# Kernel optimization log

Hardware: AMD Instinct MI355X
Metric: run time of the kernel (lower is better)

Reference implementation:

```python
import jax, jax.numpy as jnp
import numpy as np

N = 100000   # nodes
E = 1600000  # edges
D = 128      # input feature dim
H = 64       # hidden dim
G = 64       # graphs in batch


def setup_inputs() -> dict:
    key = jax.random.key(0)
    ks = jax.random.split(key, 12)
    x = jax.random.normal(ks[0], (N, D), dtype=jnp.float32)
    ei = jax.random.randint(ks[1], (2, E), 0, N, dtype=jnp.int32)
    ew = jax.random.uniform(ks[2], (E,), dtype=jnp.float32)
    b = jnp.sort(jax.random.randint(ks[3], (N,), 0, G, dtype=jnp.int32))
    s = 0.05
    W1 = jax.random.normal(ks[4], (D, H), jnp.float32) * s
    b1 = jnp.zeros((H,), jnp.float32)
    W2 = jax.random.normal(ks[5], (H, H), jnp.float32) * s
    b2 = jnp.zeros((H,), jnp.float32)
    Wm1 = jax.random.normal(ks[6], (H, 32), jnp.float32) * s
    bm1 = jnp.zeros((32,), jnp.float32)
    Wm2 = jax.random.normal(ks[7], (32, 1), jnp.float32) * s
    bm2 = jnp.zeros((1,), jnp.float32)
    return {"x": x, "ei": ei, "ew": ew, "b": b,
            "W1": W1, "b1": b1, "W2": W2, "b2": b2,
            "Wm1": Wm1, "bm1": bm1, "Wm2": Wm2, "bm2": bm2}


def _gcn_norm(ei, ew, n):
    # PyG gcn_norm with add_self_loops=True (self-loop weight 1)
    loops = jnp.arange(n, dtype=ei.dtype)
    row = jnp.concatenate([ei[0], loops])
    col = jnp.concatenate([ei[1], loops])
    w = jnp.concatenate([ew, jnp.ones((n,), ew.dtype)])
    deg = jax.ops.segment_sum(w, col, num_segments=n)
    dinv = jnp.where(deg > 0, jax.lax.rsqrt(deg), 0.0)
    norm = dinv[row] * w * dinv[col]  # [E+N]
    return row, col, norm


def _gcn_conv(x, W, bias, row, col, norm, n):
    h = x @ W                                   # [N,H] small GEMM
    msg = h[row] * norm[:, None]                # gather over edges
    return jax.ops.segment_sum(msg, col, num_segments=n) + bias


def reference(x, ei, ew, b, W1, b1, W2, b2, Wm1, bm1, Wm2, bm2):
    n = x.shape[0]
    row, col, norm = _gcn_norm(ei, ew, n)
    h = jax.nn.relu(_gcn_conv(x, W1, b1, row, col, norm, n))
    h = jax.nn.relu(_gcn_conv(h, W2, b2, row, col, norm, n))
    # global_mean_pool over batch vector b
    sums = jax.ops.segment_sum(h, b, num_segments=G)
    cnt = jax.ops.segment_sum(jnp.ones((n,), h.dtype), b, num_segments=G)
    pooled = sums / jnp.maximum(cnt, 1.0)[:, None]  # [G,H]
    # MLP head: Linear(H,32) -> ReLU -> Linear(32,1)
    return jax.nn.relu(pooled @ Wm1 + bm1) @ Wm2 + bm2
```

## Files before the change

kernel.cpp:

```cpp
#include <hip/hip_runtime.h>
#include <hip/hip_bf16.h>
#include <hip/hip_fp16.h>


#define DIMH 64
#define BSH 7
#define BSZ 128
#define NBUCK_MAX 1024
#define EPB 4096
#define ESTRIDE 3072
#define CSTRIDE 4096

typedef _Float16 v8h __attribute__((ext_vector_type(8)));
typedef float v4f __attribute__((ext_vector_type(4)));

__global__ __launch_bounds__(512) void k_part(const int* __restrict__ row,
                                              const int* __restrict__ col,
                                              const float* __restrict__ ew,
                                              int* __restrict__ cursor,
                                              unsigned long long* __restrict__ part,
                                              int E, int nbuck) {
    __shared__ int h[NBUCK_MAX];
    __shared__ int h2[NBUCK_MAX];
    __shared__ int st[NBUCK_MAX];
    for (int i = threadIdx.x; i < nbuck; i += 512) { h[i] = 0; h2[i] = 0; }
    __syncthreads();
    int ebeg = blockIdx.x * EPB;
    int eend = min(ebeg + EPB, E);
    for (int e = ebeg + threadIdx.x; e < eend; e += 512)
        atomicAdd(&h[col[e] >> BSH], 1);
    __syncthreads();
    for (int i = threadIdx.x; i < nbuck; i += 512) {
        int c = h[i];
        st[i] = c ? i * ESTRIDE + atomicAdd(&cursor[i], c) : 0;
    }
    __syncthreads();
    for (int e = ebeg + threadIdx.x; e < eend; e += 512) {
        int c = col[e];
        int b = c >> BSH;
        int r = atomicAdd(&h2[b], 1);
        int slot = st[b] + r;
        if (slot < (b + 1) * ESTRIDE) {
            unsigned long long rec =
                ((unsigned long long)__float_as_uint(ew[e]) << 32) |
                ((unsigned long long)(unsigned)row[e] << 8) |
                (unsigned)(c & (BSZ - 1));
            part[slot] = rec;
        }
    }
}

__global__ __launch_bounds__(256) void k_sortB(const unsigned long long* __restrict__ part,
                                               const int* __restrict__ cursor,
                                               int2* __restrict__ csr,
                                               unsigned* __restrict__ rp,
                                               float* __restrict__ dinv, int N) {
    __shared__ int cnt[BSZ];
    __shared__ int scn[BSZ];
    __shared__ int cur[BSZ];
    __shared__ float dg[BSZ];
    int b = blockIdx.x;
    int nb0 = b << BSH;
    int nn = min(BSZ, N - nb0);
    int tid = threadIdx.x;
    if (tid < BSZ) { cnt[tid] = 0; dg[tid] = 1.0f; }
    __syncthreads();
    int ebeg = b * ESTRIDE;
    int eend = ebeg + min(cursor[b], ESTRIDE);
    for (int e = ebeg + tid; e < eend; e += 256)
        atomicAdd(&cnt[(int)(part[e] & (BSZ - 1))], 1);
    __syncthreads();
    int pc = 0;
    if (tid < BSZ) pc = min((cnt[tid] + 15) & ~15, 496);
    if (tid < BSZ) scn[tid] = pc;
    __syncthreads();
    for (int o = 1; o < BSZ; o <<= 1) {
        int t = 0;
        if (tid >= o && tid < BSZ) t = scn[tid - o];
        __syncthreads();
        if (tid >= o && tid < BSZ) scn[tid] += t;
        __syncthreads();
    }
    int Pb = b * CSTRIDE;
    int pofs = 0;
    if (tid < BSZ) {
        pofs = scn[tid] - pc;
        cur[tid] = pofs;
        if (tid < nn)
            rp[nb0 + tid] = ((unsigned)(pc >> 4) << 26) | (unsigned)(Pb + pofs);
    }
    __syncthreads();
    for (int e = ebeg + tid; e < eend; e += 256) {
        unsigned long long rec = part[e];
        int cl = (int)(rec & (BSZ - 1));
        float w = __uint_as_float((unsigned)(rec >> 32));
        int slot = atomicAdd(&cur[cl], 1);
        csr[Pb + slot] = make_int2((int)((rec >> 8) & 0xFFFFFF), __float_as_int(w));
        atomicAdd(&dg[cl], w);
    }
    __syncthreads();
    if (tid < nn) {
        int c = min(cnt[tid], pc);
        for (int k = c; k < pc; k++)
            csr[Pb + pofs + k] = make_int2(nb0 + tid, 0);
        dinv[nb0 + tid] = rsqrtf(dg[tid]);
    }
}

__global__ __launch_bounds__(256) void k_gemm_mfma(const float* __restrict__ X,
                                                   const float* __restrict__ W,
                                                   const float* __restrict__ dinv,
                                                   __half* __restrict__ Y, int n) {
    __shared__ _Float16 Wh[128 * 64];
    int tid = threadIdx.x;
    for (int i = tid * 4; i < 128 * 64; i += 256 * 4) {
        float4 w = *(const float4*)&W[i];
        Wh[i]     = (_Float16)w.x;
        Wh[i + 1] = (_Float16)w.y;
        Wh[i + 2] = (_Float16)w.z;
        Wh[i + 3] = (_Float16)w.w;
    }
    __syncthreads();

    int wv = tid >> 6;
    int lane = tid & 63;
    int m = lane & 15;
    int quad = lane >> 4;
    int tile = blockIdx.x * 4 + wv;
    int ntiles = (n + 15) >> 4;
    if (tile >= ntiles) return;

    v8h bf[4][4];
#pragma unroll
    for (int nt = 0; nt < 4; nt++)
#pragma unroll
        for (int s = 0; s < 4; s++)
#pragma unroll
            for (int j = 0; j < 8; j++)
                bf[nt][s][j] = Wh[(s * 32 + quad * 8 + j) * 64 + nt * 16 + m];

    v4f acc[4];
#pragma unroll
    for (int nt = 0; nt < 4; nt++) acc[nt] = (v4f){0.f, 0.f, 0.f, 0.f};

    int row = min(tile * 16 + m, n - 1);
    const float* xr = X + (size_t)row * 128;
#pragma unroll
    for (int s = 0; s < 4; s++) {
        float4 lo = *(const float4*)&xr[s * 32 + quad * 8];
        float4 hi = *(const float4*)&xr[s * 32 + quad * 8 + 4];
        v8h af;
        af[0] = (_Float16)lo.x; af[1] = (_Float16)lo.y;
        af[2] = (_Float16)lo.z; af[3] = (_Float16)lo.w;
        af[4] = (_Float16)hi.x; af[5] = (_Float16)hi.y;
        af[6] = (_Float16)hi.z; af[7] = (_Float16)hi.w;
#pragma unroll
        for (int nt = 0; nt < 4; nt++)
            acc[nt] = __builtin_amdgcn_mfma_f32_16x16x32_f16(af, bf[nt][s], acc[nt], 0, 0, 0);
    }

#pragma unroll
    for (int r = 0; r < 4; r++) {
        int node = tile * 16 + quad * 4 + r;
        if (node < n) {
            float di = dinv[node];
#pragma unroll
            for (int nt = 0; nt < 4; nt++)
                Y[(size_t)node * DIMH + nt * 16 + m] = __float2half(di * acc[nt][r]);
        }
    }
}

__global__ __launch_bounds__(256) void k_agg1f(const __half* __restrict__ Hin,
                                               const unsigned* __restrict__ rp,
                                               const int2* __restrict__ csr,
                                               const float* __restrict__ dinv,
                                               const float* __restrict__ bias,
                                               const float* __restrict__ W2,
                                               __half* __restrict__ T2, int n) {
    __shared__ float W2s[DIMH * DIMH];
    __shared__ __align__(16) _Float16 hbuf[4][DIMH];
    int tid = threadIdx.x;
    for (int i = tid * 4; i < DIMH * DIMH; i += 256 * 4)
        *(float4*)&W2s[i] = *(const float4*)&W2[i];
    __syncthreads();

    int lane = tid & 63;
    int wv = tid >> 6;
    int q = lane >> 4;
    int fp = lane & 15;

    const uint2* H2 = (const uint2*)Hin;
    int ngroups = (n + 3) >> 2;
    for (int grp = blockIdx.x; grp < ngroups; grp += gridDim.x) {
        int node = grp * 4 + wv;
        if (node >= n) continue;
        unsigned pk = rp[node];
        int p = (int)(pk & 0x3FFFFFFu);
        int iters = (int)(pk >> 26);
        float a0 = 0.f, a1 = 0.f, a2 = 0.f, a3 = 0.f;
        if (q == 0) {
            uint2 su = H2[(size_t)node * 16 + fp];
            float2 f0 = __half22float2(*(__half2*)&su.x);
            float2 f1 = __half22float2(*(__half2*)&su.y);
            a0 = f0.x; a1 = f0.y; a2 = f1.x; a3 = f1.y;
        }
        int it = 0;
        for (; it + 2 <= iters; it += 2, p += 32) {
            int4 mA0 = *(const int4*)&csr[p + 2 * q];
            int4 mB0 = *(const int4*)&csr[p + 8 + 2 * q];
            int4 mA1 = *(const int4*)&csr[p + 16 + 2 * q];
            int4 mB1 = *(const int4*)&csr[p + 24 + 2 * q];
            uint2 u0 = H2[(size_t)mA0.x * 16 + fp];
            uint2 u1 = H2[(size_t)mA0.z * 16 + fp];
            uint2 u2 = H2[(size_t)mB0.x * 16 + fp];
            uint2 u3 = H2[(size_t)mB0.z * 16 + fp];
            uint2 u4 = H2[(size_t)mA1.x * 16 + fp];
            uint2 u5 = H2[(size_t)mA1.z * 16 + fp];
            uint2 u6 = H2[(size_t)mB1.x * 16 + fp];
            uint2 u7 = H2[(size_t)mB1.z * 16 + fp];
            float w0 = __int_as_float(mA0.y), w1 = __int_as_float(mA0.w);
            float w2 = __int_as_float(mB0.y), w3 = __int_as_float(mB0.w);
            float w4 = __int_as_float(mA1.y), w5 = __int_as_float(mA1.w);
            float w6 = __int_as_float(mB1.y), w7 = __int_as_float(mB1.w);
            float2 f;
            f = __half22float2(*(__half2*)&u0.x); a0 += w0 * f.x; a1 += w0 * f.y;
            f = __half22float2(*(__half2*)&u0.y); a2 += w0 * f.x; a3 += w0 * f.y;
            f = __half22float2(*(__half2*)&u1.x); a0 += w1 * f.x; a1 += w1 * f.y;
            f = __half22float2(*(__half2*)&u1.y); a2 += w1 * f.x; a3 += w1 * f.y;
            f = __half22float2(*(__half2*)&u2.x); a0 += w2 * f.x; a1 += w2 * f.y;
            f = __half22float2(*(__half2*)&u2.y); a2 += w2 * f.x; a3 += w2 * f.y;
            f = __half22float2(*(__half2*)&u3.x); a0 += w3 * f.x; a1 += w3 * f.y;
            f = __half22float2(*(__half2*)&u3.y); a2 += w3 * f.x; a3 += w3 * f.y;
            f = __half22float2(*(__half2*)&u4.x); a0 += w4 * f.x; a1 += w4 * f.y;
            f = __half22float2(*(__half2*)&u4.y); a2 += w4 * f.x; a3 += w4 * f.y;
            f = __half22float2(*(__half2*)&u5.x); a0 += w5 * f.x; a1 += w5 * f.y;
            f = __half22float2(*(__half2*)&u5.y); a2 += w5 * f.x; a3 += w5 * f.y;
            f = __half22float2(*(__half2*)&u6.x); a0 += w6 * f.x; a1 += w6 * f.y;
            f = __half22float2(*(__half2*)&u6.y); a2 += w6 * f.x; a3 += w6 * f.y;
            f = __half22float2(*(__half2*)&u7.x); a0 += w7 * f.x; a1 += w7 * f.y;
            f = __half22float2(*(__half2*)&u7.y); a2 += w7 * f.x; a3 += w7 * f.y;
        }
        if (it < iters) {
            int4 mA = *(const int4*)&csr[p + 2 * q];
            int4 mB = *(const int4*)&csr[p + 8 + 2 * q];
            uint2 u0 = H2[(size_t)mA.x * 16 + fp];
            uint2 u1 = H2[(size_t)mA.z * 16 + fp];
            uint2 u2 = H2[(size_t)mB.x * 16 + fp];
            uint2 u3 = H2[(size_t)mB.z * 16 + fp];
            float w0 = __int_as_float(mA.y), w1 = __int_as_float(mA.w);
            float w2 = __int_as_float(mB.y), w3 = __int_as_float(mB.w);
            float2 f;
            f = __half22float2(*(__half2*)&u0.x); a0 += w0 * f.x; a1 += w0 * f.y;
            f = __half22float2(*(__half2*)&u0.y); a2 += w0 * f.x; a3 += w0 * f.y;
            f = __half22float2(*(__half2*)&u1.x); a0 += w1 * f.x; a1 += w1 * f.y;
            f = __half22float2(*(__half2*)&u1.y); a2 += w1 * f.x; a3 += w1 * f.y;
            f = __half22float2(*(__half2*)&u2.x); a0 += w2 * f.x; a1 += w2 * f.y;
            f = __half22float2(*(__half2*)&u2.y); a2 += w2 * f.x; a3 += w2 * f.y;
            f = __half22float2(*(__half2*)&u3.x); a0 += w3 * f.x; a1 += w3 * f.y;
            f = __half22float2(*(__half2*)&u3.y); a2 += w3 * f.x; a3 += w3 * f.y;
        }
        a0 += __shfl_xor(a0, 16, 64); a0 += __shfl_xor(a0, 32, 64);
        a1 += __shfl_xor(a1, 16, 64); a1 += __shfl_xor(a1, 32, 64);
        a2 += __shfl_xor(a2, 16, 64); a2 += __shfl_xor(a2, 32, 64);
        a3 += __shfl_xor(a3, 16, 64); a3 += __shfl_xor(a3, 32, 64);
        float di = dinv[node];
        if (q == 0) {
            float4 bs = *(const float4*)&bias[fp * 4];
            float v0 = fmaxf(di * a0 + bs.x, 0.f);
            float v1 = fmaxf(di * a1 + bs.y, 0.f);
            float v2 = fmaxf(di * a2 + bs.z, 0.f);
            float v3 = fmaxf(di * a3 + bs.w, 0.f);
            __half2 h0 = __floats2half2_rn(v0, v1);
            __half2 h1 = __floats2half2_rn(v2, v3);
            uint2 o;
            o.x = *(unsigned*)&h0;
            o.y = *(unsigned*)&h1;
            *(uint2*)&hbuf[wv][fp * 4] = o;
        }
        float acc2 = 0.f;
        const unsigned* hb = (const unsigned*)hbuf[wv];
#pragma unroll
        for (int k8 = 0; k8 < 8; k8++) {
            uint4 hc = *(const uint4*)&hb[k8 * 4];
            float2 g0 = __half22float2(*(__half2*)&hc.x);
            float2 g1 = __half22float2(*(__half2*)&hc.y);
            float2 g2 = __half22float2(*(__half2*)&hc.z);
            float2 g3 = __half22float2(*(__half2*)&hc.w);
            const float* wc = &W2s[(k8 * 8) * DIMH + lane];
            acc2 += g0.x * wc[0 * DIMH] + g0.y * wc[1 * DIMH]
                  + g1.x * wc[2 * DIMH] + g1.y * wc[3 * DIMH]
                  + g2.x * wc[4 * DIMH] + g2.y * wc[5 * DIMH]
                  + g3.x * wc[6 * DIMH] + g3.y * wc[7 * DIMH];
        }
        T2[(size_t)node * DIMH + lane] = __float2half(di * acc2);
    }
}

__global__ __launch_bounds__(256) void k_aggN(const __half* __restrict__ Hin,
                                              const unsigned* __restrict__ rp,
                                              const int2* __restrict__ csr,
                                              const float* __restrict__ dinv,
                                              const float* __restrict__ bias,
                                              __half* __restrict__ Hout, int n) {
    int lane = threadIdx.x & 63;
    int wv = threadIdx.x >> 6;
    int node = blockIdx.x * 4 + wv;
    if (node >= n) return;
    unsigned pk = rp[node];
    int p = (int)(pk & 0x3FFFFFFu);
    int iters = (int)(pk >> 26);
    int q = lane >> 4;
    int fp = lane & 15;
    const uint2* H2 = (const uint2*)Hin;
    float a0 = 0.f, a1 = 0.f, a2 = 0.f, a3 = 0.f;
    if (q == 0) {
        uint2 su = H2[(size_t)node * 16 + fp];
        float2 f0 = __half22float2(*(__half2*)&su.x);
        float2 f1 = __half22float2(*(__half2*)&su.y);
        a0 = f0.x; a1 = f0.y; a2 = f1.x; a3 = f1.y;
    }
    int it = 0;
    for (; it + 2 <= iters; it += 2, p += 32) {
        int4 mA0 = *(const int4*)&csr[p + 2 * q];
        int4 mB0 = *(const int4*)&csr[p + 8 + 2 * q];
        int4 mA1 = *(const int4*)&csr[p + 16 + 2 * q];
        int4 mB1 = *(const int4*)&csr[p + 24 + 2 * q];
        uint2 u0 = H2[(size_t)mA0.x * 16 + fp];
        uint2 u1 = H2[(size_t)mA0.z * 16 + fp];
        uint2 u2 = H2[(size_t)mB0.x * 16 + fp];
        uint2 u3 = H2[(size_t)mB0.z * 16 + fp];
        uint2 u4 = H2[(size_t)mA1.x * 16 + fp];
        uint2 u5 = H2[(size_t)mA1.z * 16 + fp];
        uint2 u6 = H2[(size_t)mB1.x * 16 + fp];
        uint2 u7 = H2[(size_t)mB1.z * 16 + fp];
        float w0 = __int_as_float(mA0.y), w1 = __int_as_float(mA0.w);
        float w2 = __int_as_float(mB0.y), w3 = __int_as_float(mB0.w);
        float w4 = __int_as_float(mA1.y), w5 = __int_as_float(mA1.w);
        float w6 = __int_as_float(mB1.y), w7 = __int_as_float(mB1.w);
        float2 f;
        f = __half22float2(*(__half2*)&u0.x); a0 += w0 * f.x; a1 += w0 * f.y;
        f = __half22float2(*(__half2*)&u0.y); a2 += w0 * f.x; a3 += w0 * f.y;
        f = __half22float2(*(__half2*)&u1.x); a0 += w1 * f.x; a1 += w1 * f.y;
        f = __half22float2(*(__half2*)&u1.y); a2 += w1 * f.x; a3 += w1 * f.y;
        f = __half22float2(*(__half2*)&u2.x); a0 += w2 * f.x; a1 += w2 * f.y;
        f = __half22float2(*(__half2*)&u2.y); a2 += w2 * f.x; a3 += w2 * f.y;
        f = __half22float2(*(__half2*)&u3.x); a0 += w3 * f.x; a1 += w3 * f.y;
        f = __half22float2(*(__half2*)&u3.y); a2 += w3 * f.x; a3 += w3 * f.y;
        f = __half22float2(*(__half2*)&u4.x); a0 += w4 * f.x; a1 += w4 * f.y;
        f = __half22float2(*(__half2*)&u4.y); a2 += w4 * f.x; a3 += w4 * f.y;
        f = __half22float2(*(__half2*)&u5.x); a0 += w5 * f.x; a1 += w5 * f.y;
        f = __half22float2(*(__half2*)&u5.y); a2 += w5 * f.x; a3 += w5 * f.y;
        f = __half22float2(*(__half2*)&u6.x); a0 += w6 * f.x; a1 += w6 * f.y;
        f = __half22float2(*(__half2*)&u6.y); a2 += w6 * f.x; a3 += w6 * f.y;
        f = __half22float2(*(__half2*)&u7.x); a0 += w7 * f.x; a1 += w7 * f.y;
        f = __half22float2(*(__half2*)&u7.y); a2 += w7 * f.x; a3 += w7 * f.y;
    }
    if (it < iters) {
        int4 mA = *(const int4*)&csr[p + 2 * q];
        int4 mB = *(const int4*)&csr[p + 8 + 2 * q];
        uint2 u0 = H2[(size_t)mA.x * 16 + fp];
        uint2 u1 = H2[(size_t)mA.z * 16 + fp];
        uint2 u2 = H2[(size_t)mB.x * 16 + fp];
        uint2 u3 = H2[(size_t)mB.z * 16 + fp];
        float w0 = __int_as_float(mA.y), w1 = __int_as_float(mA.w);
        float w2 = __int_as_float(mB.y), w3 = __int_as_float(mB.w);
        float2 f;
        f = __half22float2(*(__half2*)&u0.x); a0 += w0 * f.x; a1 += w0 * f.y;
        f = __half22float2(*(__half2*)&u0.y); a2 += w0 * f.x; a3 += w0 * f.y;
        f = __half22float2(*(__half2*)&u1.x); a0 += w1 * f.x; a1 += w1 * f.y;
        f = __half22float2(*(__half2*)&u1.y); a2 += w1 * f.x; a3 += w1 * f.y;
        f = __half22float2(*(__half2*)&u2.x); a0 += w2 * f.x; a1 += w2 * f.y;
        f = __half22float2(*(__half2*)&u2.y); a2 += w2 * f.x; a3 += w2 * f.y;
        f = __half22float2(*(__half2*)&u3.x); a0 += w3 * f.x; a1 += w3 * f.y;
        f = __half22float2(*(__half2*)&u3.y); a2 += w3 * f.x; a3 += w3 * f.y;
    }
    a0 += __shfl_xor(a0, 16, 64); a0 += __shfl_xor(a0, 32, 64);
    a1 += __shfl_xor(a1, 16, 64); a1 += __shfl_xor(a1, 32, 64);
    a2 += __shfl_xor(a2, 16, 64); a2 += __shfl_xor(a2, 32, 64);
    a3 += __shfl_xor(a3, 16, 64); a3 += __shfl_xor(a3, 32, 64);
    if (q == 0) {
        float di = dinv[node];
        float4 bs = *(const float4*)&bias[fp * 4];
        float v0 = fmaxf(di * a0 + bs.x, 0.f);
        float v1 = fmaxf(di * a1 + bs.y, 0.f);
        float v2 = fmaxf(di * a2 + bs.z, 0.f);
        float v3 = fmaxf(di * a3 + bs.w, 0.f);
        __half2 h0 = __floats2half2_rn(v0, v1);
        __half2 h1 = __floats2half2_rn(v2, v3);
        uint2 o;
        o.x = *(unsigned*)&h0;
        o.y = *(unsigned*)&h1;
        *(uint2*)&Hout[(size_t)node * DIMH + fp * 4] = o;
    }
}

__global__ __launch_bounds__(256) void k_pool(const __half* __restrict__ Hin,
                                              const int* __restrict__ b,
                                              float* __restrict__ sums,
                                              float* __restrict__ cntG, int n) {
    const int CHUNK = 64;
    int lane = threadIdx.x & 63;
    int wave = threadIdx.x >> 6;
    int start = (blockIdx.x * 4 + wave) * CHUNK;
    if (start >= n) return;
    int end = min(start + CHUNK, n);
    float acc = 0.f;
    int g_cur = b[start];
    int cnt_local = 0;
    for (int i = start; i < end; i++) {
        int g = b[i];
        if (g != g_cur) {
            atomicAdd(&sums[g_cur * DIMH + lane], acc);
            if (lane == 0) atomicAdd(&cntG[g_cur], (float)cnt_local);
            acc = 0.f;
            cnt_local = 0;
            g_cur = g;
        }
        acc += __half2float(Hin[(size_t)i * DIMH + lane]);
        cnt_local++;
    }
    atomicAdd(&sums[g_cur * DIMH + lane], acc);
    if (lane == 0) atomicAdd(&cntG[g_cur], (float)cnt_local);
}

__global__ __launch_bounds__(64) void k_mlp(const float* __restrict__ sums,
                                            const float* __restrict__ cntG,
                                            const float* __restrict__ Wm1,
                                            const float* __restrict__ bm1,
                                            const float* __restrict__ Wm2,
                                            const float* __restrict__ bm2,
                                            float* __restrict__ out, int G) {
    int g = threadIdx.x;
    if (g >= G) return;
    float c = cntG[g];
    float inv = 1.f / (c > 1.f ? c : 1.f);
    float pooled[DIMH];
#pragma unroll
    for (int k = 0; k < DIMH; k++) pooled[k] = sums[g * DIMH + k] * inv;
    float o = 0.f;
    for (int j = 0; j < 32; j++) {
        float t = bm1[j];
#pragma unroll
        for (int k = 0; k < DIMH; k++) t += pooled[k] * Wm1[k * 32 + j];
        t = t > 0.f ? t : 0.f;
        o += t * Wm2[j];
    }
    out[g] = o + bm2[0];
}


extern "C" void kernel_launch(void* const* d_in, const int* in_sizes, int n_in,
                              void* d_out, int out_size, void* d_ws, size_t ws_size,
                              hipStream_t stream) {
    const float* x   = (const float*)d_in[0];
    const int*   ei  = (const int*)d_in[1];
    const float* ew  = (const float*)d_in[2];
    const int*   bvec= (const int*)d_in[3];
    const float* W1  = (const float*)d_in[4];
    const float* b1  = (const float*)d_in[5];
    const float* W2  = (const float*)d_in[6];
    const float* b2  = (const float*)d_in[7];
    const float* Wm1 = (const float*)d_in[8];
    const float* bm1 = (const float*)d_in[9];
    const float* Wm2 = (const float*)d_in[10];
    const float* bm2 = (const float*)d_in[11];
    float* out = (float*)d_out;

    const int E = in_sizes[2];
    const int N = in_sizes[3];
    const int G = out_size;
    const int* row = ei;
    const int* col = ei + E;
    const int nbuck = (N + BSZ - 1) >> BSH;

    char* p = (char*)d_ws;
    auto alloc = [&](size_t bytes) {
        void* r = (void*)p;
        p += (bytes + 255) & ~(size_t)255;
        return r;
    };

    unsigned long long* part = (unsigned long long*)alloc((size_t)nbuck * ESTRIDE * 8);
    int2*  csr    = (int2*)alloc((size_t)nbuck * CSTRIDE * 8);
    unsigned* rp  = (unsigned*)alloc((size_t)N * 4);
    float* dinv   = (float*)alloc((size_t)N * 4);
    __half* hA    = (__half*)alloc((size_t)N * DIMH * 2);
    __half* hB    = (__half*)alloc((size_t)N * DIMH * 2);
    int zeroInts  = nbuck + G * DIMH + G;
    int* cursor   = (int*)alloc((size_t)zeroInts * 4);
    float* sums   = (float*)(cursor + nbuck);
    float* cntG   = sums + G * DIMH;

    hipMemsetAsync(cursor, 0, (size_t)zeroInts * 4, stream);

    const int PB = (E + EPB - 1) / EPB;
    const int NT = (N + 15) / 16;

    k_part<<<PB, 512, 0, stream>>>(row, col, ew, cursor, part, E, nbuck);
    k_sortB<<<nbuck, 256, 0, stream>>>(part, cursor, csr, rp, dinv, N);

    k_gemm_mfma<<<(NT + 3) / 4, 256, 0, stream>>>(x, W1, dinv, hA, N);

    k_agg1f<<<4096, 256, 0, stream>>>(hA, rp, csr, dinv, b1, W2, hB, N);

    k_aggN<<<(N + 3) / 4, 256, 0, stream>>>(hB, rp, csr, dinv, b2, hA, N);

    k_pool<<<(N + 255) / 256, 256, 0, stream>>>(hA, bvec, sums, cntG, N);
    k_mlp<<<1, 64, 0, stream>>>(sums, cntG, Wm1, bm1, Wm2, bm2, out, G);
}
```

Baseline: 316.0 us.

## Use 32-bit byte-offset addressing, fp16 dot2 W2 transform, and occupancy hints in aggregation

The aggregation kernels now compute gather addresses as 32-bit unsigned byte offsets instead of 64-bit size_t indexing, which cuts address arithmetic and VGPR use. The fused W2 transform in k_agg1f stores a transposed, padded fp16 copy of W2 in shared memory and uses fdot2 instructions in place of fp32 FMAs, which also halves its LDS footprint. A launch_bounds minimum of 8 blocks per CU is added to push occupancy up for latency hiding. The risks are register spills under the tighter bound and lower precision from the fp16 W2 product.

Measured after the change: 312.6 us. No clear change (-1.1%).

```diff
diff --git a/kernel.cpp b/kernel.cpp
--- a/kernel.cpp
+++ b/kernel.cpp
@@ -12,6 +12,8 @@
 #define CSTRIDE 4096
 
 typedef _Float16 v8h __attribute__((ext_vector_type(8)));
+typedef _Float16 v4h __attribute__((ext_vector_type(4)));
+typedef _Float16 hv2 __attribute__((ext_vector_type(2)));
 typedef float v4f __attribute__((ext_vector_type(4)));
 
 __global__ __launch_bounds__(512) void k_part(const int* __restrict__ row,
@@ -171,18 +173,21 @@
     }
 }
 
-__global__ __launch_bounds__(256) void k_agg1f(const __half* __restrict__ Hin,
-                                               const unsigned* __restrict__ rp,
-                                               const int2* __restrict__ csr,
-                                               const float* __restrict__ dinv,
-                                               const float* __restrict__ bias,
-                                               const float* __restrict__ W2,
-                                               __half* __restrict__ T2, int n) {
-    __shared__ float W2s[DIMH * DIMH];
+__global__ __launch_bounds__(256, 8) void k_agg1f(const __half* __restrict__ Hin,
+                                                  const unsigned* __restrict__ rp,
+                                                  const int2* __restrict__ csr,
+                                                  const float* __restrict__ dinv,
+                                                  const float* __restrict__ bias,
+                                                  const float* __restrict__ W2,
+                                                  __half* __restrict__ T2, int n) {
+    __shared__ __align__(16) _Float16 W2T[64 * 68];
     __shared__ __align__(16) _Float16 hbuf[4][DIMH];
     int tid = threadIdx.x;
-    for (int i = tid * 4; i < DIMH * DIMH; i += 256 * 4)
-        *(float4*)&W2s[i] = *(const float4*)&W2[i];
+    for (int idx = tid; idx < 64 * 64; idx += 256) {
+        int k = idx >> 6;
+        int o = idx & 63;
+        W2T[o * 68 + k] = (_Float16)W2[idx];
+    }
     __syncthreads();
 
     int lane = tid & 63;
@@ -190,35 +195,37 @@
     int q = lane >> 4;
     int fp = lane & 15;
 
-    const uint2* H2 = (const uint2*)Hin;
+    const char* Hb = (const char*)Hin;
+    const char* Cb = (const char*)csr;
     int ngroups = (n + 3) >> 2;
     for (int grp = blockIdx.x; grp < ngroups; grp += gridDim.x) {
         int node = grp * 4 + wv;
         if (node >= n) continue;
         unsigned pk = rp[node];
-        int p = (int)(pk & 0x3FFFFFFu);
+        unsigned pb = ((pk & 0x3FFFFFFu) << 3) + (unsigned)(q << 4);
         int iters = (int)(pk >> 26);
         float a0 = 0.f, a1 = 0.f, a2 = 0.f, a3 = 0.f;
         if (q == 0) {
-            uint2 su = H2[(size_t)node * 16 + fp];
+            uint2 su = *(const uint2*)(Hb + (((unsigned)node << 7) + (unsigned)(fp << 3)));
             float2 f0 = __half22float2(*(__half2*)&su.x);
             float2 f1 = __half22float2(*(__half2*)&su.y);
             a0 = f0.x; a1 = f0.y; a2 = f1.x; a3 = f1.y;
         }
+        unsigned fo = (unsigned)(fp << 3);
         int it = 0;
-        for (; it + 2 <= iters; it += 2, p += 32) {
-            int4 mA0 = *(const int4*)&csr[p + 2 * q];
-            int4 mB0 = *(const int4*)&csr[p + 8 + 2 * q];
-            int4 mA1 = *(const int4*)&csr[p + 16 + 2 * q];
-            int4 mB1 = *(const int4*)&csr[p + 24 + 2 * q];
-            uint2 u0 = H2[(size_t)mA0.x * 16 + fp];
-            uint2 u1 = H2[(size_t)mA0.z * 16 + fp];
-            uint2 u2 = H2[(size_t)mB0.x * 16 + fp];
-            uint2 u3 = H2[(size_t)mB0.z * 16 + fp];
-            uint2 u4 = H2[(size_t)mA1.x * 16 + fp];
-            uint2 u5 = H2[(size_t)mA1.z * 16 + fp];
-            uint2 u6 = H2[(size_t)mB1.x * 16 + fp];
-            uint2 u7 = H2[(size_t)mB1.z * 16 + fp];
+        for (; it + 2 <= iters; it += 2, pb += 256) {
+            int4 mA0 = *(const int4*)(Cb + pb);
+            int4 mB0 = *(const int4*)(Cb + pb + 64);
+            int4 mA1 = *(const int4*)(Cb + pb + 128);
+            int4 mB1 = *(const int4*)(Cb + pb + 192);
+            uint2 u0 = *(const uint2*)(Hb + (((unsigned)mA0.x << 7) + fo));
+            uint2 u1 = *(const uint2*)(Hb + (((unsigned)mA0.z << 7) + fo));
+            uint2 u2 = *(const uint2*)(Hb + (((unsigned)mB0.x << 7) + fo));
+            uint2 u3 = *(const uint2*)(Hb + (((unsigned)mB0.z << 7) + fo));
+            uint2 u4 = *(const uint2*)(Hb + (((unsigned)mA1.x << 7) + fo));
+            uint2 u5 = *(const uint2*)(Hb + (((unsigned)mA1.z << 7) + fo));
+            uint2 u6 = *(const uint2*)(Hb + (((unsigned)mB1.x << 7) + fo));
+            uint2 u7 = *(const uint2*)(Hb + (((unsigned)mB1.z << 7) + fo));
             float w0 = __int_as_float(mA0.y), w1 = __int_as_float(mA0.w);
             float w2 = __int_as_float(mB0.y), w3 = __int_as_float(mB0.w);
             float w4 = __int_as_float(mA1.y), w5 = __int_as_float(mA1.w);
@@ -242,12 +249,12 @@
             f = __half22float2(*(__half2*)&u7.y); a2 += w7 * f.x; a3 += w7 * f.y;
         }
         if (it < iters) {
-            int4 mA = *(const int4*)&csr[p + 2 * q];
-            int4 mB = *(const int4*)&csr[p + 8 + 2 * q];
-            uint2 u0 = H2[(size_t)mA.x * 16 + fp];
-            uint2 u1 = H2[(size_t)mA.z * 16 + fp];
-            uint2 u2 = H2[(size_t)mB.x * 16 + fp];
-            uint2 u3 = H2[(size_t)mB.z * 16 + fp];
+            int4 mA = *(const int4*)(Cb + pb);
+            int4 mB = *(const int4*)(Cb + pb + 64);
+            uint2 u0 = *(const uint2*)(Hb + (((unsigned)mA.x << 7) + fo));
+            uint2 u1 = *(const uint2*)(Hb + (((unsigned)mA.z << 7) + fo));
+            uint2 u2 = *(const uint2*)(Hb + (((unsigned)mB.x << 7) + fo));
+            uint2 u3 = *(const uint2*)(Hb + (((unsigned)mB.z << 7) + fo));
             float w0 = __int_as_float(mA.y), w1 = __int_as_float(mA.w);
             float w2 = __int_as_float(mB.y), w3 = __int_as_float(mB.w);
             float2 f;
@@ -278,62 +285,64 @@
             o.y = *(unsigned*)&h1;
             *(uint2*)&hbuf[wv][fp * 4] = o;
         }
-        float acc2 = 0.f;
-        const unsigned* hb = (const unsigned*)hbuf[wv];
+        float accA = 0.f, accB = 0.f;
 #pragma unroll
         for (int k8 = 0; k8 < 8; k8++) {
-            uint4 hc = *(const uint4*)&hb[k8 * 4];
-            float2 g0 = __half22float2(*(__half2*)&hc.x);
-            float2 g1 = __half22float2(*(__half2*)&hc.y);
-            float2 g2 = __half22float2(*(__half2*)&hc.z);
-            float2 g3 = __half22float2(*(__half2*)&hc.w);
-            const float* wc = &W2s[(k8 * 8) * DIMH + lane];
-            acc2 += g0.x * wc[0 * DIMH] + g0.y * wc[1 * DIMH]
-                  + g1.x * wc[2 * DIMH] + g1.y * wc[3 * DIMH]
-                  + g2.x * wc[4 * DIMH] + g2.y * wc[5 * DIMH]
-                  + g3.x * wc[6 * DIMH] + g3.y * wc[7 * DIMH];
-        }
-        T2[(size_t)node * DIMH + lane] = __float2half(di * acc2);
-    }
-}
-
-__global__ __launch_bounds__(256) void k_aggN(const __half* __restrict__ Hin,
-                                              const unsigned* __restrict__ rp,
-                                              const int2* __restrict__ csr,
-                                              const float* __restrict__ dinv,
-                                              const float* __restrict__ bias,
-                                              __half* __restrict__ Hout, int n) {
+            v8h hv = *(const v8h*)&hbuf[wv][k8 * 8];
+            v4h wa = *(const v4h*)&W2T[lane * 68 + k8 * 8];
+            v4h wb = *(const v4h*)&W2T[lane * 68 + k8 * 8 + 4];
+            hv2 h0 = {hv[0], hv[1]}, h1 = {hv[2], hv[3]};
+            hv2 h2_ = {hv[4], hv[5]}, h3 = {hv[6], hv[7]};
+            hv2 w0 = {wa[0], wa[1]}, w1 = {wa[2], wa[3]};
+            hv2 w2_ = {wb[0], wb[1]}, w3 = {wb[2], wb[3]};
+            accA = __builtin_amdgcn_fdot2(h0, w0, accA, false);
+            accB = __builtin_amdgcn_fdot2(h1, w1, accB, false);
+            accA = __builtin_amdgcn_fdot2(h2_, w2_, accA, false);
+            accB = __builtin_amdgcn_fdot2(h3, w3, accB, false);
+        }
+        T2[(size_t)node * DIMH + lane] = __float2half(di * (accA + accB));
+    }
+}
+
+__global__ __launch_bounds__(256, 8) void k_aggN(const __half* __restrict__ Hin,
+                                                 const unsigned* __restrict__ rp,
+                                                 const int2* __restrict__ csr,
+                                                 const float* __restrict__ dinv,
+                                                 const float* __restrict__ bias,
+                                                 __half* __restrict__ Hout, int n) {
     int lane = threadIdx.x & 63;
     int wv = threadIdx.x >> 6;
     int node = blockIdx.x * 4 + wv;
     if (node >= n) return;
     unsigned pk = rp[node];
-    int p = (int)(pk & 0x3FFFFFFu);
     int iters = (int)(pk >> 26);
     int q = lane >> 4;
     int fp = lane & 15;
-    const uint2* H2 = (const uint2*)Hin;
+    unsigned pb = ((pk & 0x3FFFFFFu) << 3) + (unsigned)(q << 4);
+    unsigned fo = (unsigned)(fp << 3);
+    const char* Hb = (const char*)Hin;
+    const char* Cb = (const char*)csr;
     float a0 = 0.f, a1 = 0.f, a2 = 0.f, a3 = 0.f;
     if (q == 0) {
-        uint2 su = H2[(size_t)node * 16 + fp];
+        uint2 su = *(const uint2*)(Hb + (((unsigned)node << 7) + fo));
         float2 f0 = __half22float2(*(__half2*)&su.x);
         float2 f1 = __half22float2(*(__half2*)&su.y);
         a0 = f0.x; a1 = f0.y; a2 = f1.x; a3 = f1.y;
     }
     int it = 0;
-    for (; it + 2 <= iters; it += 2, p += 32) {
-        int4 mA0 = *(const int4*)&csr[p + 2 * q];
-        int4 mB0 = *(const int4*)&csr[p + 8 + 2 * q];
-        int4 mA1 = *(const int4*)&csr[p + 16 + 2 * q];
-        int4 mB1 = *(const int4*)&csr[p + 24 + 2 * q];
-        uint2 u0 = H2[(size_t)mA0.x * 16 + fp];
-        uint2 u1 = H2[(size_t)mA0.z * 16 + fp];
-        uint2 u2 = H2[(size_t)mB0.x * 16 + fp];
-        uint2 u3 = H2[(size_t)mB0.z * 16 + fp];
-        uint2 u4 = H2[(size_t)mA1.x * 16 + fp];
-        uint2 u5 = H2[(size_t)mA1.z * 16 + fp];
-        uint2 u6 = H2[(size_t)mB1.x * 16 + fp];
-        uint2 u7 = H2[(size_t)mB1.z * 16 + fp];
+    for (; it + 2 <= iters; it += 2, pb += 256) {
+        int4 mA0 = *(const int4*)(Cb + pb);
+        int4 mB0 = *(const int4*)(Cb + pb + 64);
+        int4 mA1 = *(const int4*)(Cb + pb + 128);
+        int4 mB1 = *(const int4*)(Cb + pb + 192);
+        uint2 u0 = *(const uint2*)(Hb + (((unsigned)mA0.x << 7) + fo));
+        uint2 u1 = *(const uint2*)(Hb + (((unsigned)mA0.z << 7) + fo));
+        uint2 u2 = *(const uint2*)(Hb + (((unsigned)mB0.x << 7) + fo));
+        uint2 u3 = *(const uint2*)(Hb + (((unsigned)mB0.z << 7) + fo));
+        uint2 u4 = *(const uint2*)(Hb + (((unsigned)mA1.x << 7) + fo));
+        uint2 u5 = *(const uint2*)(Hb + (((unsigned)mA1.z << 7) + fo));
+        uint2 u6 = *(const uint2*)(Hb + (((unsigned)mB1.x << 7) + fo));
+        uint2 u7 = *(const uint2*)(Hb + (((unsigned)mB1.z << 7) + fo));
         float w0 = __int_as_float(mA0.y), w1 = __int_as_float(mA0.w);
         float w2 = __int_as_float(mB0.y), w3 = __int_as_float(mB0.w);
         float w4 = __int_as_float(mA1.y), w5 = __int_as_float(mA1.w);
@@ -357,12 +366,12 @@
         f = __half22float2(*(__half2*)&u7.y); a2 += w7 * f.x; a3 += w7 * f.y;
     }
     if (it < iters) {
-        int4 mA = *(const int4*)&csr[p + 2 * q];
-        int4 mB = *(const int4*)&csr[p + 8 + 2 * q];
-        uint2 u0 = H2[(size_t)mA.x * 16 + fp];
-        uint2 u1 = H2[(size_t)mA.z * 16 + fp];
-        uint2 u2 = H2[(size_t)mB.x * 16 + fp];
-        uint2 u3 = H2[(size_t)mB.z * 16 + fp];
+        int4 mA = *(const int4*)(Cb + pb);
+        int4 mB = *(const int4*)(Cb + pb + 64);
+        uint2 u0 = *(const uint2*)(Hb + (((unsigned)mA.x << 7) + fo));
+        uint2 u1 = *(const uint2*)(Hb + (((unsigned)mA.z << 7) + fo));
+        uint2 u2 = *(const uint2*)(Hb + (((unsigned)mB.x << 7) + fo));
+        uint2 u3 = *(const uint2*)(Hb + (((unsigned)mB.z << 7) + fo));
         float w0 = __int_as_float(mA.y), w1 = __int_as_float(mA.w);
         float w2 = __int_as_float(mB.y), w3 = __int_as_float(mB.w);
         float2 f;
```
